# Optimization experiments

Measured on AMD Instinct MI355X. Metric: run time of the kernel, lower is better.

Reference implementation:

```python
import jax, jax.numpy as jnp
import numpy as np

H = 512          # hidden_size
E = 2 * H        # bidirectional embed dim
NH = 8           # attention heads
HD = E // NH     # head dim = 128
SEQ = 10         # hard-coded seq_len in forward
IN = 512         # input_size
OUT = 256        # output_size


def _gru_dir(gi, Whh, bhh, reverse):
    # gi: [B,S,3H] precomputed input-side gate pre-activations
    if reverse:
        gi = gi[:, ::-1]
    B = gi.shape[0]
    h0 = jnp.zeros((B, H), gi.dtype)

    def step(h, gi_t):
        gh = h @ Whh.T + bhh                      # [B,3H]
        ir, iz, inn = jnp.split(gi_t, 3, axis=-1)
        hr, hz, hn = jnp.split(gh, 3, axis=-1)
        r = jax.nn.sigmoid(ir + hr)
        z = jax.nn.sigmoid(iz + hz)
        n = jnp.tanh(inn + r * hn)
        h_new = (1.0 - z) * n + z * h
        return h_new, h_new

    _, hs = jax.lax.scan(step, h0, jnp.swapaxes(gi, 0, 1))
    hs = jnp.swapaxes(hs, 0, 1)                   # [B,S,H]
    if reverse:
        hs = hs[:, ::-1]
    return hs


def _bi_gru_layer(x_seq, Wih, Whh, bih, bhh):
    # Wih: [2, 3H, in]; dir 0 = forward, dir 1 = backward
    outs = []
    for d, rev in ((0, False), (1, True)):
        gi = jnp.einsum('bsi,gi->bsg', x_seq, Wih[d]) + bih[d]
        outs.append(_gru_dir(gi, Whh[d], bhh[d], rev))
    return jnp.concatenate(outs, axis=-1)         # [B,S,2H]


def _attention(x, in_proj_w, in_proj_b, out_proj_w, out_proj_b):
    B, S, _ = x.shape
    qkv = x @ in_proj_w.T + in_proj_b             # [B,S,3E]
    q, k, v = jnp.split(qkv, 3, axis=-1)
    q = q.reshape(B, S, NH, HD)
    k = k.reshape(B, S, NH, HD)
    v = v.reshape(B, S, NH, HD)
    scores = jnp.einsum('bqhd,bkhd->bhqk', q, k) / jnp.sqrt(jnp.asarray(HD, x.dtype))
    attn = jax.nn.softmax(scores, axis=-1)
    o = jnp.einsum('bhqk,bkhd->bqhd', attn, v).reshape(B, S, E)
    return o @ out_proj_w.T + out_proj_b


def _forward(x, Wp, bp, Wih0, Whh0, bih0, bhh0, Wih1, Whh1, bih1, bhh1,
             in_proj_w, in_proj_b, out_proj_w, out_proj_b, W1, b1, W2, b2):
    x_proj = x @ Wp.T + bp                        # [B,H]
    phases = 2.0 * np.pi * np.arange(SEQ) / SEQ
    cos = jnp.asarray(np.cos(phases), x.dtype)    # [S]
    sin = jnp.asarray(np.sin(phases), x.dtype)
    rolled = jnp.roll(x_proj, shift=1, axis=-1)
    x_seq = (x_proj[:, None, :] * (1.0 + 0.1 * cos[None, :, None])
             + 0.05 * sin[None, :, None] * rolled[:, None, :])  # [B,S,H]
    h1 = _bi_gru_layer(x_seq, Wih0, Whh0, bih0, bhh0)           # [B,S,2H]
    gru_out = _bi_gru_layer(h1, Wih1, Whh1, bih1, bhh1)         # [B,S,2H]
    attn_out = _attention(gru_out, in_proj_w, in_proj_b, out_proj_w, out_proj_b)
    aggregated = jnp.mean(gru_out + attn_out, axis=1)           # [B,2H]
    hid = jnp.tanh(aggregated @ W1.T + b1)                      # [B,128]
    return hid @ W2.T + b2                                      # [B,OUT]


def setup_inputs() -> dict:
    key = jax.random.key(0)
    ks = jax.random.split(key, 24)
    s = 1.0 / np.sqrt(H)
    u = lambda k, shape: jax.random.uniform(k, shape, jnp.float32, -s, s)
    return {
        'x': jax.random.normal(ks[0], (4096, IN), jnp.float32),
        'Wp': u(ks[1], (H, IN)), 'bp': u(ks[2], (H,)),
        'Wih0': u(ks[3], (2, 3 * H, H)), 'Whh0': u(ks[4], (2, 3 * H, H)),
        'bih0': u(ks[5], (2, 3 * H)), 'bhh0': u(ks[6], (2, 3 * H)),
        'Wih1': u(ks[7], (2, 3 * H, 2 * H)), 'Whh1': u(ks[8], (2, 3 * H, H)),
        'bih1': u(ks[9], (2, 3 * H)), 'bhh1': u(ks[10], (2, 3 * H)),
        'in_proj_w': u(ks[11], (3 * E, E)), 'in_proj_b': u(ks[12], (3 * E,)),
        'out_proj_w': u(ks[13], (E, E)), 'out_proj_b': u(ks[14], (E,)),
        'W1': u(ks[15], (128, E)), 'b1': u(ks[16], (128,)),
        'W2': u(ks[17], (OUT, 128)), 'b2': u(ks[18], (OUT,)),
    }


def reference(x, Wp, bp, Wih0, Whh0, bih0, bhh0, Wih1, Whh1, bih1, bhh1,
              in_proj_w, in_proj_b, out_proj_w, out_proj_b, W1, b1, W2, b2):
    return _forward(x, Wp, bp, Wih0, Whh0, bih0, bhh0, Wih1, Whh1, bih1, bhh1,
                    in_proj_w, in_proj_b, out_proj_w, out_proj_b, W1, b1, W2, b2)
```

## Files before the change

### kernel.cpp

```cpp
#include <hip/hip_runtime.h>
#include <math.h>


#define SEQ 10

typedef unsigned short bf16u;
typedef __attribute__((ext_vector_type(8))) short short8v;
typedef __attribute__((ext_vector_type(4))) float f32x4;

#define AS1 __attribute__((address_space(1)))
#define AS3 __attribute__((address_space(3)))

__device__ __forceinline__ float b2f(bf16u u) {
    union { unsigned int i; float f; } v; v.i = ((unsigned int)u) << 16; return v.f;
}
__device__ __forceinline__ bf16u f2b(float f) {
    union { float f; unsigned int i; } v; v.f = f;
    unsigned int r = (v.i + 0x7FFFu + ((v.i >> 16) & 1u)) >> 16;
    return (bf16u)r;
}
__device__ __forceinline__ float fast_sigm(float x) { return 1.0f / (1.0f + __expf(-x)); }
__device__ __forceinline__ float fast_tanh(float x) {
    float e = __expf(-2.0f * x);
    return 2.0f / (1.0f + e) - 1.0f;
}

__global__ void cvt_f2b(const float* __restrict__ src, bf16u* __restrict__ dst, int n4)
{
    int i = blockIdx.x * 256 + threadIdx.x;
    if (i < n4) {
        float4 v = ((const float4*)src)[i];
        ushort4 u; u.x = f2b(v.x); u.y = f2b(v.y); u.z = f2b(v.z); u.w = f2b(v.w);
        ((ushort4*)dst)[i] = u;
    }
}

template <typename TC>
__global__ __launch_bounds__(512) void gemm_mfma256(
    const bf16u* __restrict__ A, long long sAz, int lda,
    const bf16u* __restrict__ W, long long sWz,
    const float* __restrict__ bias, long long sBz,
    TC* __restrict__ C, long long sCz, int ldc,
    int K, int act)
{
    __shared__ bf16u As[2][256 * 64];
    __shared__ bf16u Ws[2][256 * 64];

    const int z = blockIdx.z;
    A += (long long)z * sAz;
    W += (long long)z * sWz;
    C += (long long)z * sCz;
    const float* bz = bias ? (bias + (long long)z * sBz) : nullptr;

    const int gx = gridDim.x;
    const int nwg = gx * gridDim.y;
    const int orig = blockIdx.y * gx + blockIdx.x;
    const int q = nwg >> 3, rres = nwg & 7;
    const int xcd = orig & 7, loc = orig >> 3;
    const int wgid = (xcd < rres ? xcd * (q + 1) : rres * (q + 1) + (xcd - rres) * q) + loc;
    const int bm = (wgid / gx) * 256;
    const int bn = (wgid % gx) * 256;

    const int tid = threadIdx.x;
    const int lane = tid & 63;
    const int w = tid >> 6;
    const int wm = w >> 2;
    const int wn = w & 3;
    const int l15 = lane & 15;
    const int lk8 = (lane >> 4) * 8;

    f32x4 acc[8][4];
#pragma unroll
    for (int i = 0; i < 8; ++i)
#pragma unroll
        for (int j = 0; j < 4; ++j)
#pragma unroll
            for (int r = 0; r < 4; ++r) acc[i][j][r] = 0.0f;

    const int srow = lane >> 3;
    const int scol = (lane & 7) * 8;
    const bf16u* Ag[4];
    const bf16u* Wg[4];
    int loff[4];
#pragma unroll
    for (int p = 0; p < 4; ++p) {
        const int r = p * 64 + w * 8 + srow;
        Ag[p] = A + (long long)(bm + r) * lda + scol;
        Wg[p] = W + (long long)(bn + r) * K + scol;
        loff[p] = (p * 8 + w) * 512;
    }

    const int nt = K >> 6;

#pragma unroll
    for (int p = 0; p < 4; ++p) {
        __builtin_amdgcn_global_load_lds((const AS1 void*)(Ag[p]),
            (AS3 void*)(&As[0][loff[p]]), 16, 0, 0);
        __builtin_amdgcn_global_load_lds((const AS1 void*)(Wg[p]),
            (AS3 void*)(&Ws[0][loff[p]]), 16, 0, 0);
    }
    __syncthreads();

    for (int t = 0; t < nt; ++t) {
        const int pb = t & 1;
        if (t + 1 < nt) {
            const int k1 = (t + 1) << 6;
#pragma unroll
            for (int p = 0; p < 4; ++p) {
                __builtin_amdgcn_global_load_lds((const AS1 void*)(Ag[p] + k1),
                    (AS3 void*)(&As[1 - pb][loff[p]]), 16, 0, 0);
                __builtin_amdgcn_global_load_lds((const AS1 void*)(Wg[p] + k1),
                    (AS3 void*)(&Ws[1 - pb][loff[p]]), 16, 0, 0);
            }
        }
#pragma unroll
        for (int ks = 0; ks < 2; ++ks) {
            short8v af[8], bfr[4];
#pragma unroll
            for (int i = 0; i < 8; ++i)
                af[i] = *(const short8v*)(&As[pb][(wm * 128 + i * 16 + l15) * 64 + ks * 32 + lk8]);
#pragma unroll
            for (int i = 0; i < 4; ++i)
                bfr[i] = *(const short8v*)(&Ws[pb][(wn * 64 + i * 16 + l15) * 64 + ks * 32 + lk8]);
#pragma unroll
            for (int mi = 0; mi < 8; ++mi)
#pragma unroll
                for (int ni = 0; ni < 4; ++ni)
                    acc[mi][ni] = __builtin_amdgcn_mfma_f32_16x16x32_bf16(
                        af[mi], bfr[ni], acc[mi][ni], 0, 0, 0);
        }
        __syncthreads();
    }

    const int r0 = (lane >> 4) * 4;
#pragma unroll
    for (int mi = 0; mi < 8; ++mi) {
#pragma unroll
        for (int ni = 0; ni < 4; ++ni) {
            const int col = bn + wn * 64 + ni * 16 + l15;
            float badd = bz ? bz[col] : 0.0f;
#pragma unroll
            for (int r = 0; r < 4; ++r) {
                const long long row = bm + wm * 128 + mi * 16 + r0 + r;
                float v = acc[mi][ni][r] + badd;
                if (act) v = tanhf(v);
                if constexpr (sizeof(TC) == 4) ((float*)C)[row * ldc + col] = v;
                else                           ((bf16u*)C)[row * ldc + col] = f2b(v);
            }
        }
    }
}

template <typename TC>
__global__ __launch_bounds__(256) void gemm_mfma(
    const bf16u* __restrict__ A, long long sAz, int lda,
    const bf16u* __restrict__ W, long long sWz,
    const float* __restrict__ bias, long long sBz,
    TC* __restrict__ C, long long sCz, int ldc,
    int K, int act)
{
    __shared__ bf16u As[128 * 64];
    __shared__ bf16u Ws[128 * 64];

    const int z = blockIdx.z;
    A += (long long)z * sAz;
    W += (long long)z * sWz;
    C += (long long)z * sCz;
    const float* bz = bias ? (bias + (long long)z * sBz) : nullptr;

    const int gx = gridDim.x;
    const int nwg = gx * gridDim.y;
    const int orig = blockIdx.y * gx + blockIdx.x;
    const int q = nwg >> 3, rres = nwg & 7;
    const int xcd = orig & 7, loc = orig >> 3;
    const int wgid = (xcd < rres ? xcd * (q + 1) : rres * (q + 1) + (xcd - rres) * q) + loc;
    const int bm = (wgid / gx) * 128;
    const int bn = (wgid % gx) * 128;

    const int tid = threadIdx.x;
    const int lane = tid & 63;
    const int wave = tid >> 6;
    const int wr = (wave >> 1) * 64;
    const int wc = (wave & 1) * 64;
    const int l15 = lane & 15;
    const int lk8 = (lane >> 4) * 8;

    f32x4 acc[4][4];
#pragma unroll
    for (int i = 0; i < 4; ++i)
#pragma unroll
        for (int j = 0; j < 4; ++j)
#pragma unroll
            for (int r = 0; r < 4; ++r) acc[i][j][r] = 0.0f;

    const int sr = wave * 32 + (lane >> 3);
    const int sc = (lane & 7) * 8;
    const bf16u* Ag = A + (long long)(bm + sr) * lda + sc;
    const bf16u* Wg = W + (long long)(bn + sr) * K + sc;
    bf16u* Al = As + wave * 32 * 64;
    bf16u* Wl = Ws + wave * 32 * 64;

    for (int k0 = 0; k0 < K; k0 += 64) {
#pragma unroll
        for (int p = 0; p < 4; ++p) {
            __builtin_amdgcn_global_load_lds(
                (const AS1 void*)(Ag + k0 + (long long)(8 * p) * lda),
                (AS3 void*)(Al + 8 * p * 64), 16, 0, 0);
            __builtin_amdgcn_global_load_lds(
                (const AS1 void*)(Wg + k0 + (long long)(8 * p) * K),
                (AS3 void*)(Wl + 8 * p * 64), 16, 0, 0);
        }
        __syncthreads();
#pragma unroll
        for (int ks = 0; ks < 2; ++ks) {
            short8v af[4], bfr[4];
#pragma unroll
            for (int i = 0; i < 4; ++i)
                af[i] = *(const short8v*)(As + (wr + i * 16 + l15) * 64 + ks * 32 + lk8);
#pragma unroll
            for (int i = 0; i < 4; ++i)
                bfr[i] = *(const short8v*)(Ws + (wc + i * 16 + l15) * 64 + ks * 32 + lk8);
#pragma unroll
            for (int mi = 0; mi < 4; ++mi)
#pragma unroll
                for (int ni = 0; ni < 4; ++ni)
                    acc[mi][ni] = __builtin_amdgcn_mfma_f32_16x16x32_bf16(
                        af[mi], bfr[ni], acc[mi][ni], 0, 0, 0);
        }
        __syncthreads();
    }

    const int r0 = (lane >> 4) * 4;
#pragma unroll
    for (int mi = 0; mi < 4; ++mi) {
#pragma unroll
        for (int ni = 0; ni < 4; ++ni) {
            const int col = bn + wc + ni * 16 + l15;
            float badd = bz ? bz[col] : 0.0f;
#pragma unroll
            for (int r = 0; r < 4; ++r) {
                const long long row = bm + wr + mi * 16 + r0 + r;
                float v = acc[mi][ni][r] + badd;
                if (act) v = tanhf(v);
                if constexpr (sizeof(TC) == 4) ((float*)C)[row * ldc + col] = v;
                else                           ((bf16u*)C)[row * ldc + col] = f2b(v);
            }
        }
    }
}

template <int LAYER, bool FIRST>
__global__ __launch_bounds__(256) void gru_step(
    const bf16u* __restrict__ Hb,
    const bf16u* __restrict__ Whh,
    const float* __restrict__ bhh,
    const bf16u* __restrict__ P0,
    const bf16u* __restrict__ P1,
    const float* __restrict__ bih,
    const bf16u* __restrict__ GIT,
    const float* __restrict__ hprev,
    float* __restrict__ hnext,
    bf16u* __restrict__ hnextb,
    bf16u* __restrict__ hout,
    int t, int CB)
{
    __shared__ bf16u As[64 * 64];
    __shared__ bf16u Ws[96 * 64];

    const int z = blockIdx.z;
    const int bn = blockIdx.x * 32;
    const int bm = blockIdx.y * 64;
    const int tid = threadIdx.x;
    const int lane = tid & 63;
    const int wave = tid >> 6;
    const int wm = wave >> 1;
    const int wn = wave & 1;
    const int l15 = lane & 15;
    const int lk8 = (lane >> 4) * 8;

    f32x4 acc[3][2];
#pragma unroll
    for (int g = 0; g < 3; ++g)
#pragma unroll
        for (int i = 0; i < 2; ++i)
#pragma unroll
            for (int r = 0; r < 4; ++r) acc[g][i][r] = 0.0f;

    if constexpr (!FIRST) {
        const bf16u* hsrc = Hb + (long long)z * CB * 512;
        const bf16u* wsrc = Whh + (long long)z * 1536 * 512;

        const int sc = (lane & 7) * 8;
        const bf16u* Ag = hsrc + (long long)(bm + 16 * wave + (lane >> 3)) * 512 + sc;
        bf16u* Al = As + 16 * wave * 64;

        const bf16u* Wg[3];
#pragma unroll
        for (int p = 0; p < 3; ++p) {
            const int lr = 24 * wave + 8 * p + (lane >> 3);
            const int g = lr >> 5, c = lr & 31;
            Wg[p] = wsrc + (long long)(g * 512 + bn + c) * 512 + sc;
        }
        bf16u* Wl = Ws + 24 * wave * 64;

        for (int k0 = 0; k0 < 512; k0 += 64) {
#pragma unroll
            for (int p = 0; p < 2; ++p)
                __builtin_amdgcn_global_load_lds(
                    (const AS1 void*)(Ag + k0 + (long long)(8 * p) * 512),
                    (AS3 void*)(Al + 8 * p * 64), 16, 0, 0);
#pragma unroll
            for (int p = 0; p < 3; ++p)
                __builtin_amdgcn_global_load_lds(
                    (const AS1 void*)(Wg[p] + k0),
                    (AS3 void*)(Wl + 8 * p * 64), 16, 0, 0);
            __syncthreads();
#pragma unroll
            for (int ks = 0; ks < 2; ++ks) {
                short8v af[2], bf[3];
#pragma unroll
                for (int mi = 0; mi < 2; ++mi)
                    af[mi] = *(const short8v*)(As + (wm * 32 + mi * 16 + l15) * 64 + ks * 32 + lk8);
#pragma unroll
                for (int g = 0; g < 3; ++g)
                    bf[g] = *(const short8v*)(Ws + (g * 32 + wn * 16 + l15) * 64 + ks * 32 + lk8);
#pragma unroll
                for (int g = 0; g < 3; ++g)
#pragma unroll
                    for (int mi = 0; mi < 2; ++mi)
                        acc[g][mi] = __builtin_amdgcn_mfma_f32_16x16x32_bf16(
                            af[mi], bf[g], acc[g][mi], 0, 0, 0);
            }
            __syncthreads();
        }
    }

    const int r0 = (lane >> 4) * 4;
    const int s = z ? (SEQ - 1 - t) : t;
    float c0 = 0.0f, c1 = 0.0f;
    if (LAYER == 0) {
        float ph = 0.6283185307179586f * (float)s;
        c0 = 1.0f + 0.1f * cosf(ph);
        c1 = 0.05f * sinf(ph);
    }

    const int j = bn + wn * 16 + l15;
    const float bh0 = bhh[z * 1536 + j];
    const float bh1 = bhh[z * 1536 + 512 + j];
    const float bh2 = bhh[z * 1536 + 1024 + j];
    float bi0 = 0, bi1 = 0, bi2 = 0;
    if (LAYER == 0) {
        bi0 = bih[z * 1536 + j];
        bi1 = bih[z * 1536 + 512 + j];
        bi2 = bih[z * 1536 + 1024 + j];
    }

#pragma unroll
    for (int mi = 0; mi < 2; ++mi) {
#pragma unroll
        for (int rr = 0; rr < 4; ++rr) {
            const int m = bm + wm * 32 + mi * 16 + r0 + rr;
            float gr = acc[0][mi][rr] + bh0;
            float gz = acc[1][mi][rr] + bh1;
            float gn = acc[2][mi][rr] + bh2;
            float ir, iz, inn;
            if (LAYER == 0) {
                const bf16u* p0 = P0 + (long long)m * 3072 + z * 1536 + j;
                const bf16u* p1 = P1 + (long long)m * 3072 + z * 1536 + j;
                ir  = c0 * b2f(p0[0])    + c1 * b2f(p1[0])    + bi0;
                iz  = c0 * b2f(p0[512])  + c1 * b2f(p1[512])  + bi1;
                inn = c0 * b2f(p0[1024]) + c1 * b2f(p1[1024]) + bi2;
            } else {
                const bf16u* gi = GIT + (((long long)z * CB + m) * SEQ + s) * 1536 + j;
                ir = b2f(gi[0]); iz = b2f(gi[512]); inn = b2f(gi[1024]);
            }
            const long long ho = ((long long)z * CB + m) * 512 + j;
            float r  = fast_sigm(ir + gr);
            float zz = fast_sigm(iz + gz);
            float n  = fast_tanh(inn + r * gn);
            float hnew;
            if constexpr (FIRST) hnew = (1.0f - zz) * n;
            else                 hnew = (1.0f - zz) * n + zz * hprev[ho];
            hnext[ho]  = hnew;
            hnextb[ho] = f2b(hnew);
            hout[((long long)m * SEQ + s) * 1024 + z * 512 + j] = f2b(hnew);
        }
    }
}

__global__ void roll_b(const bf16u* __restrict__ xp, bf16u* __restrict__ rl)
{
    int idx = blockIdx.x * 256 + threadIdx.x;
    int i = idx & 511;
    int b = idx >> 9;
    rl[(size_t)b * 512 + i] = xp[(size_t)b * 512 + ((i + 511) & 511)];
}

__global__ __launch_bounds__(128) void attn_kernel(const bf16u* __restrict__ qkv,
                                                   bf16u* __restrict__ o)
{
    const int bh = blockIdx.x;
    const int h = bh & 7;
    const int bl = bh >> 3;
    const int tid = threadIdx.x;

    __shared__ float Q[SEQ][128], Kx[SEQ][128], V[SEQ][128], Amat[SEQ][SEQ];

    const bf16u* base = qkv + (size_t)bl * SEQ * 3072 + h * 128;
#pragma unroll
    for (int s = 0; s < SEQ; ++s) {
        Q[s][tid]  = b2f(base[s * 3072 + tid]);
        Kx[s][tid] = b2f(base[s * 3072 + 1024 + tid]);
        V[s][tid]  = b2f(base[s * 3072 + 2048 + tid]);
    }
    __syncthreads();

    if (tid < SEQ * SEQ) {
        int q = tid / SEQ, k = tid % SEQ;
        float acc = 0.0f;
#pragma unroll 8
        for (int d0 = 0; d0 < 128; ++d0) acc += Q[q][d0] * Kx[k][d0];
        Amat[q][k] = acc * 0.08838834764831845f;
    }
    __syncthreads();

    if (tid < SEQ) {
        float m = -1e30f;
#pragma unroll
        for (int k = 0; k < SEQ; ++k) m = fmaxf(m, Amat[tid][k]);
        float e[SEQ], ssum = 0.0f;
#pragma unroll
        for (int k = 0; k < SEQ; ++k) { e[k] = expf(Amat[tid][k] - m); ssum += e[k]; }
        float inv = 1.0f / ssum;
#pragma unroll
        for (int k = 0; k < SEQ; ++k) Amat[tid][k] = e[k] * inv;
    }
    __syncthreads();

    bf16u* ob = o + (size_t)bl * SEQ * 1024 + h * 128;
#pragma unroll
    for (int q = 0; q < SEQ; ++q) {
        float acc = 0.0f;
#pragma unroll
        for (int k = 0; k < SEQ; ++k) acc += Amat[q][k] * V[k][tid];
        ob[q * 1024 + tid] = f2b(acc);
    }
}

__global__ void mean_kernel(const bf16u* __restrict__ go, const bf16u* __restrict__ ao,
                            bf16u* __restrict__ agg)
{
    int idx = blockIdx.x * 256 + threadIdx.x;
    int j4 = (idx & 255) * 4;
    int bl = idx >> 8;
    const bf16u* g = go + (size_t)bl * (SEQ * 1024) + j4;
    const bf16u* a = ao + (size_t)bl * (SEQ * 1024) + j4;
    float s0 = 0, s1 = 0, s2 = 0, s3 = 0;
#pragma unroll
    for (int t = 0; t < SEQ; ++t) {
        ushort4 gv = *(const ushort4*)(g + t * 1024);
        ushort4 av = *(const ushort4*)(a + t * 1024);
        s0 += b2f(gv.x) + b2f(av.x);
        s1 += b2f(gv.y) + b2f(av.y);
        s2 += b2f(gv.z) + b2f(av.z);
        s3 += b2f(gv.w) + b2f(av.w);
    }
    ushort4 u; u.x = f2b(0.1f * s0); u.y = f2b(0.1f * s1); u.z = f2b(0.1f * s2); u.w = f2b(0.1f * s3);
    *(ushort4*)(agg + (size_t)bl * 1024 + j4) = u;
}

extern "C" void kernel_launch(void* const* d_in, const int* in_sizes, int n_in,
                              void* d_out, int out_size, void* d_ws, size_t ws_size,
                              hipStream_t stream)
{
    const float* x    = (const float*)d_in[0];
    const float* Wp   = (const float*)d_in[1];
    const float* bp   = (const float*)d_in[2];
    const float* Wih0 = (const float*)d_in[3];
    const float* Whh0 = (const float*)d_in[4];
    const float* bih0 = (const float*)d_in[5];
    const float* bhh0 = (const float*)d_in[6];
    const float* Wih1 = (const float*)d_in[7];
    const float* Whh1 = (const float*)d_in[8];
    const float* bih1 = (const float*)d_in[9];
    const float* bhh1 = (const float*)d_in[10];
    const float* ipw  = (const float*)d_in[11];
    const float* ipb  = (const float*)d_in[12];
    const float* opw  = (const float*)d_in[13];
    const float* opb  = (const float*)d_in[14];
    const float* W1   = (const float*)d_in[15];
    const float* b1   = (const float*)d_in[16];
    const float* W2   = (const float*)d_in[17];
    const float* b2   = (const float*)d_in[18];
    float* out = (float*)d_out;

    const long long WOVER = 9437184LL;
    const long long WALL  = 24969216LL;
    int CB = 0;
    for (int c = 4096; c >= 128; c >>= 1)
        if (WOVER + (long long)c * 114688 <= (long long)ws_size) { CB = c; break; }
    if (CB == 0) return;
    const bool resident = (WALL + (long long)CB * 114688 <= (long long)ws_size);
    const long long WB = resident ? WALL : WOVER;
    const int CBA = CB / 2;

    bf16u* wreg = (bf16u*)d_ws;
    bf16u *Wpb, *Wih0b, *Whh0b, *Wih1b, *Whh1b, *ipwb, *opwb, *W1b, *W2b;
    if (resident) {
        Wpb   = wreg;
        Wih0b = wreg + 262144;
        Whh0b = wreg + 1835008;
        Wih1b = wreg + 3407872;
        Whh1b = wreg + 6553600;
        ipwb  = wreg + 8126464;
        opwb  = wreg + 11272192;
        W1b   = wreg + 12320768;
        W2b   = wreg + 12451840;
    } else {
        Wpb   = wreg;
        Wih0b = wreg + 262144;
        Whh0b = wreg + 1835008;
        Wih1b = wreg;
        Whh1b = wreg + 3145728;
        ipwb  = wreg;
        opwb  = wreg + 3145728;
        W1b   = wreg + 4194304;
        W2b   = wreg + 4325376;
    }

    char* A0 = (char*)d_ws + WB;
    bf16u* H1c = (bf16u*)A0;
    bf16u* GOc = (bf16u*)(A0 + 20480LL * CB);
    char*  U   = A0 + 40960LL * CB;
    bf16u* P0    = (bf16u*)U;
    bf16u* P1    = (bf16u*)(U + 6144LL * CB);
    bf16u* XB    = (bf16u*)(U + 12288LL * CB);
    bf16u* XPb   = (bf16u*)(U + 13312LL * CB);
    bf16u* RLb   = (bf16u*)(U + 14336LL * CB);
    bf16u* GIT   = (bf16u*)U;
    char*  HC    = U + 61440LL * CB;
    bf16u* QKV   = (bf16u*)U;
    bf16u* OC    = (bf16u*)(U + 61440LL * CB);
    bf16u* AOC   = (bf16u*)A0;
    bf16u* AGGb  = (bf16u*)(A0 + 10240LL * CB);
    bf16u* HIDb  = (bf16u*)(A0 + 12288LL * CB);

    const dim3 blk(256);
    const int MB = CB / 128;

    auto cvt = [&](const float* s, bf16u* d, long long nfloats) {
        int n4 = (int)(nfloats / 4);
        cvt_f2b<<<(n4 + 255) / 256, blk, 0, stream>>>(s, d, n4);
    };

    if (resident) {
        cvt(Wp,   Wpb,   512LL * 512);
        cvt(Wih0, Wih0b, 2LL * 1536 * 512);
        cvt(Whh0, Whh0b, 2LL * 1536 * 512);
        cvt(Wih1, Wih1b, 2LL * 1536 * 1024);
        cvt(Whh1, Whh1b, 2LL * 1536 * 512);
        cvt(ipw,  ipwb,  3072LL * 1024);
        cvt(opw,  opwb,  1024LL * 1024);
        cvt(W1,   W1b,   128LL * 1024);
        cvt(W2,   W2b,   256LL * 128);
    }

    for (int c0 = 0; c0 < 4096; c0 += CB) {
        cvt(x + (long long)c0 * 512, XB, (long long)CB * 512);
        if (!resident) {
            cvt(Wp,   Wpb,   512LL * 512);
            cvt(Wih0, Wih0b, 2LL * 1536 * 512);
            cvt(Whh0, Whh0b, 2LL * 1536 * 512);
        }

        gemm_mfma<bf16u><<<dim3(4, MB, 1), blk, 0, stream>>>(
            XB, 0, 512, Wpb, 0, bp, 0, XPb, 0, 512, 512, 0);
        roll_b<<<CB * 2, blk, 0, stream>>>(XPb, RLb);
        gemm_mfma<bf16u><<<dim3(24, MB, 2), blk, 0, stream>>>(
            XPb, (long long)CB * 512, 512, Wih0b, 0, nullptr, 0,
            P0, (long long)CB * 3072, 3072, 512, 0);

        for (int t = 0; t < SEQ; ++t) {
            const int rb = t & 1;
            float* hprev  = (float*)(HC + (long long)rb * 6144 * CB);
            bf16u* Hbr    = (bf16u*)(HC + (long long)rb * 6144 * CB + 4096LL * CB);
            float* hnext  = (float*)(HC + (long long)(1 - rb) * 6144 * CB);
            bf16u* hnextb = (bf16u*)(HC + (long long)(1 - rb) * 6144 * CB + 4096LL * CB);
            if (t == 0)
                gru_step<0, true><<<dim3(16, CB / 64, 2), blk, 0, stream>>>(
                    Hbr, Whh0b, bhh0, P0, P1, bih0, nullptr,
                    hprev, hnext, hnextb, H1c, t, CB);
            else
                gru_step<0, false><<<dim3(16, CB / 64, 2), blk, 0, stream>>>(
                    Hbr, Whh0b, bhh0, P0, P1, bih0, nullptr,
                    hprev, hnext, hnextb, H1c, t, CB);
        }

        if (!resident) {
            cvt(Wih1, Wih1b, 2LL * 1536 * 1024);
            cvt(Whh1, Whh1b, 2LL * 1536 * 512);
        }
        gemm_mfma256<bf16u><<<dim3(6, CB * 10 / 256, 2), dim3(512), 0, stream>>>(
            H1c, 0, 1024, Wih1b, 1536LL * 1024, bih1, 1536,
            GIT, (long long)CB * SEQ * 1536, 1536, 1024, 0);

        for (int t = 0; t < SEQ; ++t) {
            const int rb = t & 1;
            float* hprev  = (float*)(HC + (long long)rb * 6144 * CB);
            bf16u* Hbr    = (bf16u*)(HC + (long long)rb * 6144 * CB + 4096LL * CB);
            float* hnext  = (float*)(HC + (long long)(1 - rb) * 6144 * CB);
            bf16u* hnextb = (bf16u*)(HC + (long long)(1 - rb) * 6144 * CB + 4096LL * CB);
            if (t == 0)
                gru_step<1, true><<<dim3(16, CB / 64, 2), blk, 0, stream>>>(
                    Hbr, Whh1b, bhh1, nullptr, nullptr, nullptr, GIT,
                    hprev, hnext, hnextb, GOc, t, CB);
            else
                gru_step<1, false><<<dim3(16, CB / 64, 2), blk, 0, stream>>>(
                    Hbr, Whh1b, bhh1, nullptr, nullptr, nullptr, GIT,
                    hprev, hnext, hnextb, GOc, t, CB);
        }

        if (!resident) {
            cvt(ipw, ipwb, 3072LL * 1024);
            cvt(opw, opwb, 1024LL * 1024);
            cvt(W1,  W1b,  128LL * 1024);
            cvt(W2,  W2b,  256LL * 128);
        }
        gemm_mfma256<bf16u><<<dim3(12, CB * 10 / 256, 1), dim3(512), 0, stream>>>(
            GOc, 0, 1024, ipwb, 0, ipb, 0, QKV, 0, 3072, 1024, 0);
        for (int a0 = 0; a0 < CB; a0 += CBA) {
            attn_kernel<<<CBA * 8, dim3(128), 0, stream>>>(
                QKV + (long long)a0 * 30720, OC);
            gemm_mfma<bf16u><<<dim3(8, CBA * 10 / 128, 1), blk, 0, stream>>>(
                OC, 0, 1024, opwb, 0, opb, 0, AOC, 0, 1024, 1024, 0);
            mean_kernel<<<CBA, blk, 0, stream>>>(
                GOc + (long long)a0 * 10240, AOC, AGGb + (long long)a0 * 1024);
        }
        gemm_mfma<bf16u><<<dim3(1, MB, 1), blk, 0, stream>>>(
            AGGb, 0, 1024, W1b, 0, b1, 0, HIDb, 0, 128, 1024, 1);
        gemm_mfma<float><<<dim3(2, MB, 1), blk, 0, stream>>>(
            HIDb, 0, 128, W2b, 0, b2, 0, out + (long long)c0 * 256, 0, 256, 128, 0);
    }
}
```

Before: 2.302 ms.

## Prefetch two K-tiles ahead with partial vmcnt waits in GEMM and GRU step

The main GEMM loop now issues loads for the first two K-tiles up front. Each iteration waits only on the older tile's loads via a partial vmcnt count and raw barriers, so the next tile's global-to-LDS copy stays in flight during the MFMA work. The GRU recurrent step kernel gets the same treatment: its single LDS buffer becomes double-buffered, replacing the load-sync-compute-sync serial loop. This is meant to hide global memory latency, at the cost of twice the LDS in gru_step and hand-counted waitcnt values that must exactly match the number of loads issued per stage.

Result: no change. 2.276 ms (-1.2%).

```diff
diff --git a/kernel.cpp b/kernel.cpp
--- a/kernel.cpp
+++ b/kernel.cpp
@@ -90,38 +90,26 @@
         loff[p] = (p * 8 + w) * 512;
     }
 
-    const int nt = K >> 6;
-
-#pragma unroll
-    for (int p = 0; p < 4; ++p) {
-        __builtin_amdgcn_global_load_lds((const AS1 void*)(Ag[p]),
-            (AS3 void*)(&As[0][loff[p]]), 16, 0, 0);
-        __builtin_amdgcn_global_load_lds((const AS1 void*)(Wg[p]),
-            (AS3 void*)(&Ws[0][loff[p]]), 16, 0, 0);
-    }
-    __syncthreads();
-
-    for (int t = 0; t < nt; ++t) {
-        const int pb = t & 1;
-        if (t + 1 < nt) {
-            const int k1 = (t + 1) << 6;
-#pragma unroll
-            for (int p = 0; p < 4; ++p) {
-                __builtin_amdgcn_global_load_lds((const AS1 void*)(Ag[p] + k1),
-                    (AS3 void*)(&As[1 - pb][loff[p]]), 16, 0, 0);
-                __builtin_amdgcn_global_load_lds((const AS1 void*)(Wg[p] + k1),
-                    (AS3 void*)(&Ws[1 - pb][loff[p]]), 16, 0, 0);
-            }
-        }
+    auto stage = [&](int kt, int b) {
+        const long long k1 = (long long)kt << 6;
+#pragma unroll
+        for (int p = 0; p < 4; ++p) {
+            __builtin_amdgcn_global_load_lds((const AS1 void*)(Ag[p] + k1),
+                (AS3 void*)(&As[b][loff[p]]), 16, 0, 0);
+            __builtin_amdgcn_global_load_lds((const AS1 void*)(Wg[p] + k1),
+                (AS3 void*)(&Ws[b][loff[p]]), 16, 0, 0);
+        }
+    };
+    auto compute = [&](int b) {
 #pragma unroll
         for (int ks = 0; ks < 2; ++ks) {
             short8v af[8], bfr[4];
 #pragma unroll
             for (int i = 0; i < 8; ++i)
-                af[i] = *(const short8v*)(&As[pb][(wm * 128 + i * 16 + l15) * 64 + ks * 32 + lk8]);
+                af[i] = *(const short8v*)(&As[b][(wm * 128 + i * 16 + l15) * 64 + ks * 32 + lk8]);
 #pragma unroll
             for (int i = 0; i < 4; ++i)
-                bfr[i] = *(const short8v*)(&Ws[pb][(wn * 64 + i * 16 + l15) * 64 + ks * 32 + lk8]);
+                bfr[i] = *(const short8v*)(&Ws[b][(wn * 64 + i * 16 + l15) * 64 + ks * 32 + lk8]);
 #pragma unroll
             for (int mi = 0; mi < 8; ++mi)
 #pragma unroll
@@ -129,8 +117,25 @@
                     acc[mi][ni] = __builtin_amdgcn_mfma_f32_16x16x32_bf16(
                         af[mi], bfr[ni], acc[mi][ni], 0, 0, 0);
         }
-        __syncthreads();
-    }
+    };
+
+    const int nt = K >> 6;
+
+    stage(0, 0);
+    stage(1, 1);
+
+    for (int t = 0; t < nt - 1; ++t) {
+        asm volatile("s_waitcnt vmcnt(8)" ::: "memory");
+        __builtin_amdgcn_s_barrier();
+        asm volatile("" ::: "memory");
+        compute(t & 1);
+        asm volatile("" ::: "memory");
+        __builtin_amdgcn_s_barrier();
+        if (t + 2 < nt) stage(t + 2, t & 1);
+    }
+    asm volatile("s_waitcnt vmcnt(0)" ::: "memory");
+    __builtin_amdgcn_s_barrier();
+    compute((nt - 1) & 1);
 
     const int r0 = (lane >> 4) * 4;
 #pragma unroll
@@ -264,8 +269,8 @@
     bf16u* __restrict__ hout,
     int t, int CB)
 {
-    __shared__ bf16u As[64 * 64];
-    __shared__ bf16u Ws[96 * 64];
+    __shared__ bf16u As[2][64 * 64];
+    __shared__ bf16u Ws[2][96 * 64];
 
     const int z = blockIdx.z;
     const int bn = blockIdx.x * 32;
@@ -292,8 +297,6 @@
 
         const int sc = (lane & 7) * 8;
         const bf16u* Ag = hsrc + (long long)(bm + 16 * wave + (lane >> 3)) * 512 + sc;
-        bf16u* Al = As + 16 * wave * 64;
-
         const bf16u* Wg[3];
 #pragma unroll
         for (int p = 0; p < 3; ++p) {
@@ -301,29 +304,30 @@
             const int g = lr >> 5, c = lr & 31;
             Wg[p] = wsrc + (long long)(g * 512 + bn + c) * 512 + sc;
         }
-        bf16u* Wl = Ws + 24 * wave * 64;
-
-        for (int k0 = 0; k0 < 512; k0 += 64) {
+
+        auto stage = [&](int kt, int b) {
+            const long long k0 = (long long)kt << 6;
 #pragma unroll
             for (int p = 0; p < 2; ++p)
                 __builtin_amdgcn_global_load_lds(
                     (const AS1 void*)(Ag + k0 + (long long)(8 * p) * 512),
-                    (AS3 void*)(Al + 8 * p * 64), 16, 0, 0);
+                    (AS3 void*)(&As[b][(16 * wave + 8 * p) * 64]), 16, 0, 0);
 #pragma unroll
             for (int p = 0; p < 3; ++p)
                 __builtin_amdgcn_global_load_lds(
                     (const AS1 void*)(Wg[p] + k0),
-                    (AS3 void*)(Wl + 8 * p * 64), 16, 0, 0);
-            __syncthreads();
+                    (AS3 void*)(&Ws[b][(24 * wave + 8 * p) * 64]), 16, 0, 0);
+        };
+        auto compute = [&](int b) {
 #pragma unroll
             for (int ks = 0; ks < 2; ++ks) {
                 short8v af[2], bf[3];
 #pragma unroll
                 for (int mi = 0; mi < 2; ++mi)
-                    af[mi] = *(const short8v*)(As + (wm * 32 + mi * 16 + l15) * 64 + ks * 32 + lk8);
+                    af[mi] = *(const short8v*)(&As[b][(wm * 32 + mi * 16 + l15) * 64 + ks * 32 + lk8]);
 #pragma unroll
                 for (int g = 0; g < 3; ++g)
-                    bf[g] = *(const short8v*)(Ws + (g * 32 + wn * 16 + l15) * 64 + ks * 32 + lk8);
+                    bf[g] = *(const short8v*)(&Ws[b][(g * 32 + wn * 16 + l15) * 64 + ks * 32 + lk8]);
 #pragma unroll
                 for (int g = 0; g < 3; ++g)
 #pragma unroll
@@ -331,8 +335,22 @@
                         acc[g][mi] = __builtin_amdgcn_mfma_f32_16x16x32_bf16(
                             af[mi], bf[g], acc[g][mi], 0, 0, 0);
             }
-            __syncthreads();
-        }
+        };
+
+        stage(0, 0);
+        stage(1, 1);
+        for (int kt = 0; kt < 7; ++kt) {
+            asm volatile("s_waitcnt vmcnt(5)" ::: "memory");
+            __builtin_amdgcn_s_barrier();
+            asm volatile("" ::: "memory");
+            compute(kt & 1);
+            asm volatile("" ::: "memory");
+            __builtin_amdgcn_s_barrier();
+            if (kt + 2 < 8) stage(kt + 2, kt & 1);
+        }
+        asm volatile("s_waitcnt vmcnt(0)" ::: "memory");
+        __builtin_amdgcn_s_barrier();
+        compute(1);
     }
 
     const int r0 = (lane >> 4) * 4;
```
